# Kernel tuning notes

Measured on AMD Instinct MI355X. Metric: run time of the kernel, lower is better.

## Reference

```python
import jax, jax.numpy as jnp
import numpy as np

EMBED_DIM = 1024
N_HEADS = 16
B, L = 2, 2048


def setup_inputs() -> dict:
    key = jax.random.key(0)
    ks = jax.random.split(key, 7)
    D = EMBED_DIM
    s = 1.0 / np.sqrt(D)
    return {
        "inputs": jax.random.normal(ks[0], (B, L, D), dtype=jnp.float32),
        "rotation_params": jax.random.normal(ks[1], (D, D), dtype=jnp.float32) * s,
        "entangle_params": jax.random.uniform(ks[2], (N_HEADS,), dtype=jnp.float32, minval=0.5, maxval=1.5),
        "Wq": jax.random.normal(ks[3], (D, D), dtype=jnp.float32) * s,
        "Wk": jax.random.normal(ks[4], (D, D), dtype=jnp.float32) * s,
        "Wv": jax.random.normal(ks[5], (D, D), dtype=jnp.float32) * s,
        "Wo": jax.random.normal(ks[6], (D, D), dtype=jnp.float32) * s,
    }


def reference(inputs, rotation_params, entangle_params, Wq, Wk, Wv, Wo):
    Bq, Lq, D = inputs.shape
    H = N_HEADS
    hd = D // H
    # Linear (no bias, torch convention x @ W.T) followed by rotation matmul
    Q = (inputs @ Wq.T) @ rotation_params
    K = (inputs @ Wk.T) @ rotation_params
    V = (inputs @ Wv.T) @ rotation_params
    # split heads: (B, H, L, hd)
    Q = Q.reshape(Bq, Lq, H, hd).transpose(0, 2, 1, 3)
    K = K.reshape(Bq, Lq, H, hd).transpose(0, 2, 1, 3)
    V = V.reshape(Bq, Lq, H, hd).transpose(0, 2, 1, 3)
    scale = entangle_params.reshape(1, H, 1, 1) / jnp.sqrt(jnp.asarray(hd, dtype=inputs.dtype))
    scores = jnp.einsum("bhqd,bhkd->bhqk", Q, K) * scale
    attn = jax.nn.softmax(scores, axis=-1)  # dropout inert (eval / p=0)
    out = jnp.einsum("bhqk,bhkd->bhqd", attn, V)
    out = out.transpose(0, 2, 1, 3).reshape(Bq, Lq, D)
    return out @ Wo.T
```

## Files before the change

kernel.cpp:

```cpp
#include <hip/hip_runtime.h>
#include <cstdint>
#include <cstddef>

typedef __attribute__((ext_vector_type(8))) short  bf16x8;
typedef __attribute__((ext_vector_type(8))) _Float16 f16x8;
typedef __attribute__((ext_vector_type(4))) _Float16 f16x4;
typedef __attribute__((ext_vector_type(4))) float  f32x4;
typedef __attribute__((ext_vector_type(4))) unsigned short u16x4;
typedef __attribute__((ext_vector_type(2))) unsigned int u32x2;

#define LOG2E 1.44269504088896340736f
#define PBIAS 6.0f

__device__ __forceinline__ unsigned short f2bf(float f) {
  unsigned int u = __builtin_bit_cast(unsigned int, f);
  u += 0x7fffu + ((u >> 16) & 1u);
  return (unsigned short)(u >> 16);
}
__device__ __forceinline__ float bf2f(unsigned short s) {
  unsigned int u = ((unsigned int)s) << 16;
  return __builtin_bit_cast(float, u);
}

__device__ __forceinline__ float fast_exp2(float x) {
  return __builtin_amdgcn_exp2f(x);
}

__device__ __forceinline__ void gll16(const void* g, void* l) {
  __builtin_amdgcn_global_load_lds(
      (const __attribute__((address_space(1))) unsigned int*)g,
      (__attribute__((address_space(3))) unsigned int*)l, 16, 0, 0);
}

__global__ __launch_bounds__(256) void prep(
    const float* __restrict__ x,  unsigned short* __restrict__ xb,
    const float* __restrict__ Wo, unsigned short* __restrict__ Wob,
    const float* __restrict__ R,  const float* __restrict__ Wq,
    const float* __restrict__ Wk, const float* __restrict__ Wv,
    unsigned short* __restrict__ RT,  unsigned short* __restrict__ WqT,
    unsigned short* __restrict__ WkT, unsigned short* __restrict__ WvT) {
  int bid = blockIdx.x;
  __shared__ unsigned short s[64][68];
  if (bid < 5120) {
    const float* src = bid < 4096 ? x : Wo;
    unsigned short* dst = bid < 4096 ? xb : Wob;
    int i = (bid < 4096 ? bid : bid - 4096) * 256 + threadIdx.x;
    float4 v = ((const float4*)src)[i];
    u16x4 o;
    o[0] = f2bf(v.x); o[1] = f2bf(v.y); o[2] = f2bf(v.z); o[3] = f2bf(v.w);
    ((u16x4*)dst)[i] = o;
    return;
  }
  int t = bid - 5120;
  int z = t >> 8, tile = t & 255;
  const float* in = z == 0 ? R : (z == 1 ? Wq : (z == 2 ? Wk : Wv));
  unsigned short* out = z == 0 ? RT : (z == 1 ? WqT : (z == 2 ? WkT : WvT));
  int r0 = (tile >> 4) * 64, c0 = (tile & 15) * 64;
  int tt = threadIdx.x;
  int tr = tt >> 4, tc4 = (tt & 15) * 4;
  for (int i = 0; i < 4; ++i) {
    int r = tr + i * 16;
    float4 v = *(const float4*)(in + (size_t)(r0 + r) * 1024 + c0 + tc4);
    s[r][tc4 + 0] = f2bf(v.x); s[r][tc4 + 1] = f2bf(v.y);
    s[r][tc4 + 2] = f2bf(v.z); s[r][tc4 + 3] = f2bf(v.w);
  }
  __syncthreads();
  for (int i = 0; i < 4; ++i) {
    int oc = tr + i * 16;
    u16x4 o;
    o[0] = s[tc4 + 0][oc]; o[1] = s[tc4 + 1][oc];
    o[2] = s[tc4 + 2][oc]; o[3] = s[tc4 + 3][oc];
    *(u16x4*)(out + (size_t)(c0 + oc) * 1024 + r0 + tc4) = o;
  }
}

template <bool BF16OUT, bool VOUT>
__global__ __launch_bounds__(256) void gemm_nt(
    const unsigned short* __restrict__ A,
    const unsigned short* __restrict__ B0, const unsigned short* __restrict__ B1,
    const unsigned short* __restrict__ B2,
    void* __restrict__ C0, void* __restrict__ C1, void* __restrict__ C2,
    int M, int N, int K) {
  const unsigned short* B = blockIdx.z == 0 ? B0 : (blockIdx.z == 1 ? B1 : B2);
  void* Cv = blockIdx.z == 0 ? C0 : (blockIdx.z == 1 ? C1 : C2);

  __shared__ unsigned short As[2][64 * 64];
  __shared__ unsigned short Bs[2][128 * 64];

  int tid = threadIdx.x, w = tid >> 6, lane = tid & 63;
  int lo = lane & 15, quad = lane >> 4;
  int m0 = blockIdx.y * 64, n0 = blockIdx.x * 128;
  int wm = (w >> 1) * 32, wn = (w & 1) * 64;

  f32x4 z4 = {0.f, 0.f, 0.f, 0.f};
  f32x4 acc[2][4];
  for (int mi = 0; mi < 2; ++mi)
    for (int ni = 0; ni < 4; ++ni) acc[mi][ni] = z4;

  int rloc = lane >> 3;
  int srcChunk = (lane & 7) ^ (rloc & 7);
  int acb = w * 2;
  int bcb = w * 4;
  const unsigned short* Ag = A + (size_t)(m0 + acb * 8 + rloc) * K + srcChunk * 8;
  const unsigned short* Bg = B + (size_t)(n0 + bcb * 8 + rloc) * K + srcChunk * 8;
  int ldsA = acb * 512 + lane * 8;
  int ldsB = bcb * 512 + lane * 8;
  int cx0 = (quad ^ (lane & 7)) * 8;
  int cx1 = ((quad + 4) ^ (lane & 7)) * 8;

#pragma unroll
  for (int j = 0; j < 2; ++j)
    gll16(Ag + (size_t)j * 8 * K, As[0] + ldsA + j * 512);
#pragma unroll
  for (int j = 0; j < 4; ++j)
    gll16(Bg + (size_t)j * 8 * K, Bs[0] + ldsB + j * 512);

  int nk = K >> 6;
  for (int kt = 0; kt < nk; ++kt) {
    int buf = kt & 1;
    __syncthreads();
    if (kt + 1 < nk) {
      int k0 = (kt + 1) << 6;
#pragma unroll
      for (int j = 0; j < 2; ++j)
        gll16(Ag + (size_t)j * 8 * K + k0, As[buf ^ 1] + ldsA + j * 512);
#pragma unroll
      for (int j = 0; j < 4; ++j)
        gll16(Bg + (size_t)j * 8 * K + k0, Bs[buf ^ 1] + ldsB + j * 512);
    }
    const unsigned short* Ab = As[buf];
    const unsigned short* Bb = Bs[buf];
#pragma unroll
    for (int ks = 0; ks < 2; ++ks) {
      int cx = ks ? cx1 : cx0;
      bf16x8 af[2], bfr[4];
#pragma unroll
      for (int mi = 0; mi < 2; ++mi)
        af[mi] = *(const bf16x8*)(Ab + (wm + mi * 16 + lo) * 64 + cx);
#pragma unroll
      for (int ni = 0; ni < 4; ++ni)
        bfr[ni] = *(const bf16x8*)(Bb + (wn + ni * 16 + lo) * 64 + cx);
#pragma unroll
      for (int mi = 0; mi < 2; ++mi)
#pragma unroll
        for (int ni = 0; ni < 4; ++ni)
          acc[mi][ni] = __builtin_amdgcn_mfma_f32_16x16x32_bf16(af[mi], bfr[ni], acc[mi][ni], 0, 0, 0);
    }
  }

  if (VOUT && blockIdx.z == 2) {
    unsigned short* Vt = (unsigned short*)Cv;
#pragma unroll
    for (int mi = 0; mi < 2; ++mi) {
      int rb = m0 + wm + ((mi >> 1) << 5) + 8 * quad + 4 * (mi & 1);
#pragma unroll
      for (int ni = 0; ni < 4; ++ni) {
        u16x4 o;
#pragma unroll
        for (int i = 0; i < 4; ++i) {
          _Float16 h = (_Float16)acc[mi][ni][i];
          o[i] = __builtin_bit_cast(unsigned short, h);
        }
        int c = n0 + wn + ni * 16 + lo;
        *(u16x4*)(Vt + (size_t)c * 4096 + rb) = o;
      }
    }
    return;
  }

#pragma unroll
  for (int mi = 0; mi < 2; ++mi)
#pragma unroll
    for (int ni = 0; ni < 4; ++ni)
      for (int i = 0; i < 4; ++i) {
        int r = m0 + wm + mi * 16 + quad * 4 + i;
        int c = n0 + wn + ni * 16 + lo;
        if (BF16OUT)
          ((unsigned short*)Cv)[(size_t)r * N + c] = f2bf(acc[mi][ni][i]);
        else
          ((float*)Cv)[(size_t)r * N + c] = acc[mi][ni][i];
      }
}

__global__ __launch_bounds__(512, 4) void flash_attn(
    const unsigned short* __restrict__ Q, const unsigned short* __restrict__ Kg_,
    const unsigned short* __restrict__ Vt, const float* __restrict__ ent,
    unsigned short* __restrict__ O) {
  int tid = threadIdx.x, w = tid >> 6, lane = tid & 63;
  int lo = lane & 15, quad = lane >> 4;
  int half = w >> 2, wl = w & 3;

  int bid = blockIdx.x;
  int g = (bid & 7) + 8 * (bid >> 7);
  int qt = (bid >> 3) & 15;
  int b = g >> 4, h = g & 15;
  int q0 = qt * 128;
  float scale = ent[h] * (0.125f * LOG2E);

  __shared__ unsigned short lds[32768];

  bf16x8 aq[2][2];
#pragma unroll
  for (int f = 0; f < 2; ++f)
#pragma unroll
    for (int ks = 0; ks < 2; ++ks) {
      uint4 v = *(const uint4*)(Q + (size_t)(b * 2048 + q0 + wl * 32 + f * 16 + lo) * 1024 +
                                h * 64 + ks * 32 + quad * 8);
      unsigned int* pv = (unsigned int*)&v;
      uint4 o; unsigned int* po = (unsigned int*)&o;
#pragma unroll
      for (int j = 0; j < 4; ++j) {
        float f0 = bf2f((unsigned short)(pv[j] & 0xffffu)) * scale;
        float f1 = bf2f((unsigned short)(pv[j] >> 16)) * scale;
        po[j] = (unsigned int)f2bf(f0) | ((unsigned int)f2bf(f1) << 16);
      }
      aq[f][ks] = *(bf16x8*)&o;
    }

  f32x4 binit = {-PBIAS, -PBIAS, -PBIAS, -PBIAS};
  f32x4 z4 = {0.f, 0.f, 0.f, 0.f};
  f32x4 acco[4][2];
#pragma unroll
  for (int di = 0; di < 4; ++di) {
    acco[di][0] = z4; acco[di][1] = z4;
  }
  float lsum0 = 0.f, lsum1 = 0.f;

  int rloc = lane >> 3;
  int srcChunk = (lane & 7) ^ (rloc & 7);
  int cb = wl * 2;
  const unsigned short* Kp = Kg_ + (size_t)(b * 2048 + half * 1024) * 1024 + h * 64;
  const unsigned short* Vp = Vt + (size_t)(h * 64) * 4096 + (size_t)(b * 2048 + half * 1024);
  int cx0 = (quad ^ (lane & 7)) * 8;
  int cx1 = ((quad + 4) ^ (lane & 7)) * 8;

  unsigned short* Kh = lds + half * 2 * 4096;
  unsigned short* Vh = lds + 16384 + half * 2 * 4096;

#pragma unroll
  for (int j = 0; j < 2; ++j) {
    int c = cb + j;
    int r = c * 8 + rloc;
    gll16(Kp + (size_t)r * 1024 + srcChunk * 8, Kh + c * 512 + lane * 8);
    gll16(Vp + (size_t)r * 4096 + srcChunk * 8, Vh + c * 512 + lane * 8);
  }

  for (int it = 0; it < 16; ++it) {
    int buf = it & 1;
    __syncthreads();
    if (it + 1 < 16) {
      int kvn = (it + 1) * 64;
#pragma unroll
      for (int j = 0; j < 2; ++j) {
        int c = cb + j;
        int r = c * 8 + rloc;
        gll16(Kp + (size_t)(kvn + r) * 1024 + srcChunk * 8, Kh + (buf ^ 1) * 4096 + c * 512 + lane * 8);
        gll16(Vp + (size_t)r * 4096 + kvn + srcChunk * 8, Vh + (buf ^ 1) * 4096 + c * 512 + lane * 8);
      }
    }
    const unsigned short* Kb_ = Kh + buf * 4096;
    const unsigned short* Vb_ = Vh + buf * 4096;

    f32x4 accs[4][2];
    __builtin_amdgcn_s_setprio(1);
#pragma unroll
    for (int kt = 0; kt < 4; ++kt) {
      bf16x8 kf0 = *(const bf16x8*)(Kb_ + (kt * 16 + lo) * 64 + cx0);
      bf16x8 kf1 = *(const bf16x8*)(Kb_ + (kt * 16 + lo) * 64 + cx1);
#pragma unroll
      for (int f = 0; f < 2; ++f) {
        f32x4 a = __builtin_amdgcn_mfma_f32_16x16x32_bf16(kf0, aq[f][0], binit, 0, 0, 0);
        accs[kt][f] = __builtin_amdgcn_mfma_f32_16x16x32_bf16(kf1, aq[f][1], a, 0, 0, 0);
      }
    }
    __builtin_amdgcn_s_setprio(0);

    f16x4 ap[4][2];
#pragma unroll
    for (int kt = 0; kt < 4; ++kt) {
#pragma unroll
      for (int f = 0; f < 2; ++f) {
        float p0 = fast_exp2(accs[kt][f][0]);
        float p1 = fast_exp2(accs[kt][f][1]);
        float p2 = fast_exp2(accs[kt][f][2]);
        float p3 = fast_exp2(accs[kt][f][3]);
        if (f == 0) lsum0 += (p0 + p1) + (p2 + p3);
        else        lsum1 += (p0 + p1) + (p2 + p3);
        u32x2 uu;
        uu[0] = __builtin_bit_cast(unsigned int, __builtin_amdgcn_cvt_pkrtz(p0, p1));
        uu[1] = __builtin_bit_cast(unsigned int, __builtin_amdgcn_cvt_pkrtz(p2, p3));
        ap[kt][f] = __builtin_bit_cast(f16x4, uu);
      }
    }

    __builtin_amdgcn_s_setprio(1);
#pragma unroll
    for (int t2 = 0; t2 < 2; ++t2) {
      f16x8 a80 = __builtin_shufflevector(ap[2 * t2][0], ap[2 * t2 + 1][0], 0, 1, 2, 3, 4, 5, 6, 7);
      f16x8 a81 = __builtin_shufflevector(ap[2 * t2][1], ap[2 * t2 + 1][1], 0, 1, 2, 3, 4, 5, 6, 7);
#pragma unroll
      for (int di = 0; di < 4; ++di) {
        f16x8 bv8 = *(const f16x8*)(Vb_ + (di * 16 + lo) * 64 +
                                    (((t2 * 4 + quad) ^ (lo & 7)) << 3));
        acco[di][0] = __builtin_amdgcn_mfma_f32_16x16x32_f16(a80, bv8, acco[di][0], 0, 0, 0);
        acco[di][1] = __builtin_amdgcn_mfma_f32_16x16x32_f16(a81, bv8, acco[di][1], 0, 0, 0);
      }
    }
    __builtin_amdgcn_s_setprio(0);
  }

  __syncthreads();
  float* cm = (float*)lds;
  float* base = cm + wl * 2304;
  if (half == 1) {
#pragma unroll
    for (int di = 0; di < 4; ++di)
#pragma unroll
      for (int f = 0; f < 2; ++f)
#pragma unroll
        for (int i = 0; i < 4; ++i)
          base[(di * 8 + f * 4 + i) * 64 + lane] = acco[di][f][i];
    base[32 * 64 + lane] = lsum0;
    base[33 * 64 + lane] = lsum1;
  }
  __syncthreads();
  if (half == 1) return;

#pragma unroll
  for (int di = 0; di < 4; ++di)
#pragma unroll
    for (int f = 0; f < 2; ++f)
#pragma unroll
      for (int i = 0; i < 4; ++i)
        acco[di][f][i] += base[(di * 8 + f * 4 + i) * 64 + lane];
  lsum0 += base[32 * 64 + lane];
  lsum1 += base[33 * 64 + lane];

#pragma unroll
  for (int f = 0; f < 2; ++f) {
    float v = f == 0 ? lsum0 : lsum1;
    v += __shfl_xor(v, 16);
    v += __shfl_xor(v, 32);
    float inv = 1.0f / v;

#pragma unroll
    for (int i = 0; i < 4; ++i) {
      float invq = __shfl(inv, quad * 4 + i);
#pragma unroll
      for (int di = 0; di < 4; ++di) {
        size_t ofs = (size_t)(b * 2048 + q0 + wl * 32 + f * 16 + quad * 4 + i) * 1024 +
                     h * 64 + di * 16 + lo;
        O[ofs] = f2bf(acco[di][f][i] * invq);
      }
    }
  }
}

extern "C" void kernel_launch(void* const* d_in, const int* in_sizes, int n_in,
                              void* d_out, int out_size, void* d_ws, size_t ws_size,
                              hipStream_t stream) {
  const float* x   = (const float*)d_in[0];
  const float* R   = (const float*)d_in[1];
  const float* ent = (const float*)d_in[2];
  const float* Wq  = (const float*)d_in[3];
  const float* Wk  = (const float*)d_in[4];
  const float* Wv  = (const float*)d_in[5];
  const float* Wo  = (const float*)d_in[6];
  float* out = (float*)d_out;

  const size_t MLD = (size_t)4096 * 1024;
  const size_t DD  = (size_t)1024 * 1024;
  if (ws_size < (MLD * 6 + DD * 8) * 2) return;

  unsigned short* ws  = (unsigned short*)d_ws;
  unsigned short* xb  = ws;
  unsigned short* RT  = xb + MLD;
  unsigned short* WqT = RT + DD;
  unsigned short* WkT = WqT + DD;
  unsigned short* WvT = WkT + DD;
  unsigned short* Wob = WvT + DD;
  unsigned short* AqT = Wob + DD;
  unsigned short* AkT = AqT + DD;
  unsigned short* AvT = AkT + DD;
  unsigned short* Qb  = AvT + DD;
  unsigned short* Kb  = Qb + MLD;
  unsigned short* Vb  = Kb + MLD;
  unsigned short* Vtf = Vb + MLD;
  unsigned short* aO  = Vtf + MLD;

  prep<<<dim3(6144), dim3(256), 0, stream>>>(
      x, xb, Wo, Wob, R, Wq, Wk, Wv, RT, WqT, WkT, WvT);

  gemm_nt<true, false><<<dim3(8, 16, 3), dim3(256), 0, stream>>>(
      RT, WqT, WkT, WvT, (void*)AqT, (void*)AkT, (void*)AvT, 1024, 1024, 1024);
  gemm_nt<true, true><<<dim3(8, 64, 3), dim3(256), 0, stream>>>(
      xb, AqT, AkT, AvT, (void*)Qb, (void*)Kb, (void*)Vtf, 4096, 1024, 1024);
  flash_attn<<<dim3(512), dim3(512), 0, stream>>>(Qb, Kb, Vtf, ent, aO);
  gemm_nt<false, false><<<dim3(8, 64, 1), dim3(256), 0, stream>>>(
      aO, Wob, Wob, Wob, (void*)out, (void*)out, (void*)out, 4096, 1024, 1024);
}
```

Measured before the change: 195.9 us.

## Load K fragments directly from global memory and shrink LDS footprint

The attention kernel stops staging K tiles in LDS and has each wave read its K MFMA fragments straight from global memory at the start of every iteration. Only V stays double-buffered in LDS, so the shared array is reduced and launch_bounds raises the occupancy hint from 4 to 6. The P fragment packing is also reorganised to build f16x8 operands directly. The trade is K loads that are exposed in global-memory latency, with no async prefetch, against lower LDS use and higher occupancy; register pressure may rise to fit the tighter bound.

```diff
diff --git a/kernel.cpp b/kernel.cpp
--- a/kernel.cpp
+++ b/kernel.cpp
@@ -182,7 +182,7 @@
       }
 }
 
-__global__ __launch_bounds__(512, 4) void flash_attn(
+__global__ __launch_bounds__(512, 6) void flash_attn(
     const unsigned short* __restrict__ Q, const unsigned short* __restrict__ Kg_,
     const unsigned short* __restrict__ Vt, const float* __restrict__ ent,
     unsigned short* __restrict__ O) {
@@ -197,7 +197,7 @@
   int q0 = qt * 128;
   float scale = ent[h] * (0.125f * LOG2E);
 
-  __shared__ unsigned short lds[32768];
+  __shared__ unsigned short lds[18432];
 
   bf16x8 aq[2][2];
 #pragma unroll
@@ -231,81 +231,81 @@
   int cb = wl * 2;
   const unsigned short* Kp = Kg_ + (size_t)(b * 2048 + half * 1024) * 1024 + h * 64;
   const unsigned short* Vp = Vt + (size_t)(h * 64) * 4096 + (size_t)(b * 2048 + half * 1024);
-  int cx0 = (quad ^ (lane & 7)) * 8;
-  int cx1 = ((quad + 4) ^ (lane & 7)) * 8;
-
-  unsigned short* Kh = lds + half * 2 * 4096;
-  unsigned short* Vh = lds + 16384 + half * 2 * 4096;
+
+  unsigned short* Vh = lds + half * 2 * 4096;
 
 #pragma unroll
   for (int j = 0; j < 2; ++j) {
     int c = cb + j;
     int r = c * 8 + rloc;
-    gll16(Kp + (size_t)r * 1024 + srcChunk * 8, Kh + c * 512 + lane * 8);
     gll16(Vp + (size_t)r * 4096 + srcChunk * 8, Vh + c * 512 + lane * 8);
   }
 
   for (int it = 0; it < 16; ++it) {
     int buf = it & 1;
     __syncthreads();
+
+    const unsigned short* Kit = Kp + (size_t)(it * 64) * 1024;
+    bf16x8 kf[4][2];
+#pragma unroll
+    for (int kt = 0; kt < 4; ++kt) {
+      kf[kt][0] = *(const bf16x8*)(Kit + (size_t)(kt * 16 + lo) * 1024 + quad * 8);
+      kf[kt][1] = *(const bf16x8*)(Kit + (size_t)(kt * 16 + lo) * 1024 + 32 + quad * 8);
+    }
+
     if (it + 1 < 16) {
       int kvn = (it + 1) * 64;
 #pragma unroll
       for (int j = 0; j < 2; ++j) {
         int c = cb + j;
         int r = c * 8 + rloc;
-        gll16(Kp + (size_t)(kvn + r) * 1024 + srcChunk * 8, Kh + (buf ^ 1) * 4096 + c * 512 + lane * 8);
         gll16(Vp + (size_t)r * 4096 + kvn + srcChunk * 8, Vh + (buf ^ 1) * 4096 + c * 512 + lane * 8);
       }
     }
-    const unsigned short* Kb_ = Kh + buf * 4096;
     const unsigned short* Vb_ = Vh + buf * 4096;
 
     f32x4 accs[4][2];
     __builtin_amdgcn_s_setprio(1);
 #pragma unroll
-    for (int kt = 0; kt < 4; ++kt) {
-      bf16x8 kf0 = *(const bf16x8*)(Kb_ + (kt * 16 + lo) * 64 + cx0);
-      bf16x8 kf1 = *(const bf16x8*)(Kb_ + (kt * 16 + lo) * 64 + cx1);
+    for (int kt = 0; kt < 4; ++kt)
 #pragma unroll
       for (int f = 0; f < 2; ++f) {
-        f32x4 a = __builtin_amdgcn_mfma_f32_16x16x32_bf16(kf0, aq[f][0], binit, 0, 0, 0);
-        accs[kt][f] = __builtin_amdgcn_mfma_f32_16x16x32_bf16(kf1, aq[f][1], a, 0, 0, 0);
-      }
-    }
+        f32x4 a = __builtin_amdgcn_mfma_f32_16x16x32_bf16(kf[kt][0], aq[f][0], binit, 0, 0, 0);
+        accs[kt][f] = __builtin_amdgcn_mfma_f32_16x16x32_bf16(kf[kt][1], aq[f][1], a, 0, 0, 0);
+      }
     __builtin_amdgcn_s_setprio(0);
 
-    f16x4 ap[4][2];
-#pragma unroll
-    for (int kt = 0; kt < 4; ++kt) {
+    f16x8 ap8[2][2];
+#pragma unroll
+    for (int t2 = 0; t2 < 2; ++t2)
 #pragma unroll
       for (int f = 0; f < 2; ++f) {
-        float p0 = fast_exp2(accs[kt][f][0]);
-        float p1 = fast_exp2(accs[kt][f][1]);
-        float p2 = fast_exp2(accs[kt][f][2]);
-        float p3 = fast_exp2(accs[kt][f][3]);
-        if (f == 0) lsum0 += (p0 + p1) + (p2 + p3);
-        else        lsum1 += (p0 + p1) + (p2 + p3);
-        u32x2 uu;
-        uu[0] = __builtin_bit_cast(unsigned int, __builtin_amdgcn_cvt_pkrtz(p0, p1));
-        uu[1] = __builtin_bit_cast(unsigned int, __builtin_amdgcn_cvt_pkrtz(p2, p3));
-        ap[kt][f] = __builtin_bit_cast(f16x4, uu);
-      }
-    }
+        uint4 uu; unsigned int* pu = (unsigned int*)&uu;
+#pragma unroll
+        for (int hkt = 0; hkt < 2; ++hkt) {
+          int kt = 2 * t2 + hkt;
+          float p0 = fast_exp2(accs[kt][f][0]);
+          float p1 = fast_exp2(accs[kt][f][1]);
+          float p2 = fast_exp2(accs[kt][f][2]);
+          float p3 = fast_exp2(accs[kt][f][3]);
+          if (f == 0) lsum0 += (p0 + p1) + (p2 + p3);
+          else        lsum1 += (p0 + p1) + (p2 + p3);
+          pu[hkt * 2]     = __builtin_bit_cast(unsigned int, __builtin_amdgcn_cvt_pkrtz(p0, p1));
+          pu[hkt * 2 + 1] = __builtin_bit_cast(unsigned int, __builtin_amdgcn_cvt_pkrtz(p2, p3));
+        }
+        ap8[t2][f] = __builtin_bit_cast(f16x8, uu);
+      }
 
     __builtin_amdgcn_s_setprio(1);
 #pragma unroll
-    for (int t2 = 0; t2 < 2; ++t2) {
-      f16x8 a80 = __builtin_shufflevector(ap[2 * t2][0], ap[2 * t2 + 1][0], 0, 1, 2, 3, 4, 5, 6, 7);
-      f16x8 a81 = __builtin_shufflevector(ap[2 * t2][1], ap[2 * t2 + 1][1], 0, 1, 2, 3, 4, 5, 6, 7);
+    for (int t2 = 0; t2 < 2; ++t2)
 #pragma unroll
       for (int di = 0; di < 4; ++di) {
         f16x8 bv8 = *(const f16x8*)(Vb_ + (di * 16 + lo) * 64 +
                                     (((t2 * 4 + quad) ^ (lo & 7)) << 3));
-        acco[di][0] = __builtin_amdgcn_mfma_f32_16x16x32_f16(a80, bv8, acco[di][0], 0, 0, 0);
-        acco[di][1] = __builtin_amdgcn_mfma_f32_16x16x32_f16(a81, bv8, acco[di][1], 0, 0, 0);
-      }
-    }
+        acco[di][0] = __builtin_amdgcn_mfma_f32_16x16x32_f16(ap8[t2][0], bv8, acco[di][0], 0, 0, 0);
+        acco[di][1] = __builtin_amdgcn_mfma_f32_16x16x32_f16(ap8[t2][1], bv8, acco[di][1], 0, 0, 0);
+      }
     __builtin_amdgcn_s_setprio(0);
   }
 
```

After: 339.7 us. +73.4%, slower.
